# Kernel optimization log

Hardware: AMD Instinct MI355X
Metric: run time of the kernel (lower is better)

## Reference

```python
import jax, jax.numpy as jnp
import numpy as np

N, D, H = 4096, 128, 8

def setup_inputs() -> dict:
    key = jax.random.key(0)
    ks = jax.random.split(key, 7)
    xavier = float(np.sqrt(6.0 / (D + D)))  # xavier_uniform for [*, D, D]
    x = jax.random.normal(ks[0], (N, D), dtype=jnp.float32)
    W_k = jax.random.uniform(ks[1], (H, D, D), minval=-xavier, maxval=xavier, dtype=jnp.float32)
    W_q = jax.random.uniform(ks[2], (H, D, D), minval=-xavier, maxval=xavier, dtype=jnp.float32)
    W_v = jax.random.uniform(ks[3], (H, D, D), minval=-xavier, maxval=xavier, dtype=jnp.float32)
    W_m = jnp.ones((H,), dtype=jnp.float32)
    lim = float(1.0 / np.sqrt(D))  # default torch Linear init range
    Wg = jax.random.uniform(ks[4], (D, D), minval=-lim, maxval=lim, dtype=jnp.float32)
    bg = jax.random.uniform(ks[5], (D,), minval=-lim, maxval=lim, dtype=jnp.float32)
    return {"x": x, "W_k": W_k, "W_q": W_q, "W_v": W_v, "W_m": W_m, "Wg": Wg, "bg": bg}

def reference(x, W_k, W_q, W_v, W_m, Wg, bg):
    # per-head projections: [H, N, D]
    q = jnp.einsum('nf,hfd->hnd', x, W_q)
    k = jnp.einsum('nf,hfd->hnd', x, W_k)
    v = jnp.einsum('nf,hfd->hnd', x, W_v)
    # dense all-pairs attention scores per head: [H, N, N]
    e = jnp.einsum('hnd,hmd->hnm', q, k)
    attn = jax.nn.softmax(e, axis=-1)
    # weighted sum over values, then head-scaled accumulation: [N, D]
    out = jnp.einsum('h,hnm,hmd->nd', W_m, attn, v)
    # residual MLP: x + ReLU(Linear(x + out))
    h = x + out
    g = jax.nn.relu(h @ Wg.T + bg)
    return x + g
```

## Files before the change

kernel.cpp:

```cpp
#include <hip/hip_runtime.h>

#define NROWS 4096
#define DDIM  128
#define NHEAD 8

typedef __attribute__((ext_vector_type(8))) short    short8;
typedef __attribute__((ext_vector_type(8))) _Float16 half8;
typedef __attribute__((ext_vector_type(4))) float    floatx4;

__device__ __forceinline__ float bf2f(unsigned short u){
  unsigned v = ((unsigned)u) << 16;
  return __builtin_bit_cast(float, v);
}
__device__ __forceinline__ unsigned short f2bf(float f){
  unsigned u = __builtin_bit_cast(unsigned, f);
  u += 0x7FFFu + ((u >> 16) & 1u);
  return (unsigned short)(u >> 16);
}
__device__ __forceinline__ void split2(float v, unsigned short& hi, unsigned short& lo){
  hi = f2bf(v);
  lo = f2bf(v - bf2f(hi));
}
__device__ __forceinline__ void async_cp16(const _Float16* g, _Float16* l){
  __builtin_amdgcn_global_load_lds(
      (const __attribute__((address_space(1))) void*)g,
      (__attribute__((address_space(3))) void*)l, 16, 0, 0);
}

__global__ void fill_kernel(float* __restrict__ out, float val, int n){
  int i = blockIdx.x * 256 + threadIdx.x;
  if (i < n) out[i] = val;
}

__global__ __launch_bounds__(256, 2) void proj_kernel(
    const float* __restrict__ x,
    const float* __restrict__ Wk, const float* __restrict__ Wv,
    _Float16* __restrict__ kfo, _Float16* __restrict__ vfo)
{
  __shared__ alignas(16) unsigned short wthi[DDIM][72];
  __shared__ alignas(16) unsigned short wtlo[DDIM][72];
  const int tid = threadIdx.x, lane = tid & 63, wave = tid >> 6;
  const int l4 = lane & 15, quad = lane >> 4;
  const int h = blockIdx.y, z = blockIdx.z;
  const float* W = (z == 0 ? Wk : Wv) + h * DDIM * DDIM;

  floatx4 acc[4][8];
#pragma unroll
  for (int t4 = 0; t4 < 4; t4++)
#pragma unroll
    for (int c = 0; c < 8; c++) acc[t4][c] = (floatx4)0.f;

  for (int fh = 0; fh < 2; fh++) {
    for (int i = tid; i < DDIM * 64; i += 256) {
      const int d = i >> 6, fl = i & 63;
      unsigned short hi, lo;
      split2(W[(fh * 64 + fl) * DDIM + d], hi, lo);
      wthi[d][fl] = hi; wtlo[d][fl] = lo;
    }
    __syncthreads();

#pragma unroll
    for (int t4 = 0; t4 < 4; t4++) {
      const int tile = blockIdx.x * 4 + t4;
      const float* xr = x + (size_t)(tile * 64 + wave * 16 + l4) * DDIM + fh * 64 + quad * 8;
      short8 ah[2], al[2];
#pragma unroll
      for (int t2 = 0; t2 < 2; t2++) {
        float4 v0 = *(const float4*)(xr + t2 * 32);
        float4 v1 = *(const float4*)(xr + t2 * 32 + 4);
        float xv[8] = {v0.x, v0.y, v0.z, v0.w, v1.x, v1.y, v1.z, v1.w};
#pragma unroll
        for (int j = 0; j < 8; j++) {
          unsigned short hi, lo; split2(xv[j], hi, lo);
          ah[t2][j] = (short)hi; al[t2][j] = (short)lo;
        }
      }
#pragma unroll
      for (int t2 = 0; t2 < 2; t2++) {
#pragma unroll
        for (int c = 0; c < 8; c++) {
          short8 bh = *(const short8*)(&wthi[c * 16 + l4][t2 * 32 + quad * 8]);
          short8 bl = *(const short8*)(&wtlo[c * 16 + l4][t2 * 32 + quad * 8]);
          acc[t4][c] = __builtin_amdgcn_mfma_f32_16x16x32_bf16(ah[t2], bh, acc[t4][c], 0, 0, 0);
          acc[t4][c] = __builtin_amdgcn_mfma_f32_16x16x32_bf16(al[t2], bh, acc[t4][c], 0, 0, 0);
          acc[t4][c] = __builtin_amdgcn_mfma_f32_16x16x32_bf16(ah[t2], bl, acc[t4][c], 0, 0, 0);
        }
      }
    }
    __syncthreads();
  }

  const int rb = wave * 16 + quad * 4;
#pragma unroll
  for (int t4 = 0; t4 < 4; t4++) {
    const int tile = blockIdx.x * 4 + t4;
    const size_t tilebase = (size_t)(h * 64 + tile) * 8192;
#pragma unroll
    for (int c = 0; c < 8; c++) {
      const int d = c * 16 + l4;
#pragma unroll
      for (int r = 0; r < 4; r++) {
        const int kl = rb + r;
        const float val = acc[t4][c][r];
        if (z == 0) {
          const int c2 = kl >> 4, l4k = kl & 15;
          const int tt = d >> 5, qd = (d >> 3) & 3, jj = d & 7;
          const int qX = qd ^ ((l4k >> 1) & 3);
          kfo[tilebase + (size_t)((c2 * 4 + tt) * 16 + l4k) * 32 + qX * 8 + jj] =
              (_Float16)val;
        } else {
          const int c2 = d >> 4, l4v = d & 15;
          const int tt = kl >> 5, qd = (kl >> 3) & 3, jj = kl & 7;
          const int qX = qd ^ ((l4v >> 1) & 3);
          vfo[tilebase + (size_t)((c2 * 2 + tt) * 16 + l4v) * 32 + qX * 8 + jj] =
              (_Float16)val;
        }
      }
    }
  }
}

union FlashLds {
  struct { unsigned short hi[DDIM][72], lo[DDIM][72]; } wq;
  float qf[64][132];
  struct { _Float16 k[2][8192], p[4][2][1024]; } kv;
};

__global__ __launch_bounds__(256, 2) void flash_kernel(
    const float* __restrict__ x, const float* __restrict__ Wq,
    const _Float16* __restrict__ kfo, const _Float16* __restrict__ vfo,
    _Float16* __restrict__ op, float* __restrict__ mb, float* __restrict__ lb)
{
  __shared__ alignas(16) FlashLds lds;
  const int tid = threadIdx.x, lane = tid & 63, wave = tid >> 6;
  const int l4 = lane & 15, quad = lane >> 4;
  const int h = blockIdx.x & 7, qt = (blockIdx.x >> 3) & 31, s = blockIdx.x >> 8;
  const int q0 = qt * 128;

  half8 aq[2][4];

  {
    floatx4 qacc[2][8];
#pragma unroll
    for (int sp = 0; sp < 2; sp++)
#pragma unroll
      for (int c = 0; c < 8; c++) qacc[sp][c] = (floatx4)0.f;

    const float* Wqh = Wq + h * DDIM * DDIM;
    for (int fh = 0; fh < 2; fh++) {
      for (int i = tid; i < DDIM * 64; i += 256) {
        const int d = i >> 6, fl = i & 63;
        unsigned short hi, lo;
        split2(Wqh[(fh * 64 + fl) * DDIM + d], hi, lo);
        lds.wq.hi[d][fl] = hi; lds.wq.lo[d][fl] = lo;
      }
      __syncthreads();
#pragma unroll
      for (int sp = 0; sp < 2; sp++) {
        const float* xr = x + (size_t)(q0 + sp * 64 + wave * 16 + l4) * DDIM + fh * 64 + quad * 8;
        short8 ah[2], al[2];
#pragma unroll
        for (int t2 = 0; t2 < 2; t2++) {
          float4 v0 = *(const float4*)(xr + t2 * 32);
          float4 v1 = *(const float4*)(xr + t2 * 32 + 4);
          float xv[8] = {v0.x, v0.y, v0.z, v0.w, v1.x, v1.y, v1.z, v1.w};
#pragma unroll
          for (int j = 0; j < 8; j++) {
            unsigned short hi, lo; split2(xv[j], hi, lo);
            ah[t2][j] = (short)hi; al[t2][j] = (short)lo;
          }
        }
#pragma unroll
        for (int t2 = 0; t2 < 2; t2++) {
#pragma unroll
          for (int c = 0; c < 8; c++) {
            short8 bh = *(const short8*)(&lds.wq.hi[c * 16 + l4][t2 * 32 + quad * 8]);
            short8 bl = *(const short8*)(&lds.wq.lo[c * 16 + l4][t2 * 32 + quad * 8]);
            qacc[sp][c] = __builtin_amdgcn_mfma_f32_16x16x32_bf16(ah[t2], bh, qacc[sp][c], 0, 0, 0);
            qacc[sp][c] = __builtin_amdgcn_mfma_f32_16x16x32_bf16(al[t2], bh, qacc[sp][c], 0, 0, 0);
            qacc[sp][c] = __builtin_amdgcn_mfma_f32_16x16x32_bf16(ah[t2], bl, qacc[sp][c], 0, 0, 0);
          }
        }
      }
      __syncthreads();
    }

#pragma unroll
    for (int sp = 0; sp < 2; sp++) {
#pragma unroll
      for (int c = 0; c < 8; c++)
#pragma unroll
        for (int r = 0; r < 4; r++)
          lds.qf[wave * 16 + quad * 4 + r][c * 16 + l4] = qacc[sp][c][r];
      __syncthreads();
      if ((wave >> 1) == sp) {
#pragma unroll
        for (int g = 0; g < 2; g++)
#pragma unroll
          for (int t = 0; t < 4; t++) {
            const float* qr = &lds.qf[(wave & 1) * 32 + g * 16 + l4][t * 32 + quad * 8];
            float4 v0 = *(const float4*)qr;
            float4 v1 = *(const float4*)(qr + 4);
            aq[g][t][0] = (_Float16)v0.x; aq[g][t][1] = (_Float16)v0.y;
            aq[g][t][2] = (_Float16)v0.z; aq[g][t][3] = (_Float16)v0.w;
            aq[g][t][4] = (_Float16)v1.x; aq[g][t][5] = (_Float16)v1.y;
            aq[g][t][6] = (_Float16)v1.z; aq[g][t][7] = (_Float16)v1.w;
          }
      }
      __syncthreads();
    }
  }

  float m_run[2][4];
#pragma unroll
  for (int g = 0; g < 2; g++)
#pragma unroll
    for (int r = 0; r < 4; r++) m_run[g][r] = -1e30f;
  floatx4 Oacc[2][8], lacc[2];
#pragma unroll
  for (int g = 0; g < 2; g++) {
    lacc[g] = (floatx4)0.f;
#pragma unroll
    for (int c = 0; c < 8; c++) Oacc[g][c] = (floatx4)0.f;
  }

  half8 vones;
#pragma unroll
  for (int j = 0; j < 8; j++) vones[j] = (_Float16)1.f;

  const _Float16* kfo_h = kfo + (size_t)h * 64 * 8192;
  const _Float16* vfo_h = vfo + (size_t)h * 64 * 8192;
  const int lq = (l4 * 4 + (quad ^ ((l4 >> 1) & 3))) * 8;
  const int kt0 = s * 32, kt1 = kt0 + 32;

  {
    const _Float16* ks = kfo_h + (size_t)kt0 * 8192 + wave * 2048 + lane * 8;
    _Float16* kd = &lds.kv.k[0][wave * 2048];
#pragma unroll
    for (int it = 0; it < 4; it++) async_cp16(ks + it * 512, kd + it * 512);
  }

  for (int kt = kt0; kt < kt1; ++kt) {
    const int cur = kt & 1;
    __syncthreads();

    half8 vfrag[8][2];
    {
      const _Float16* vtb = vfo_h + (size_t)kt * 8192;
#pragma unroll
      for (int c = 0; c < 8; c++)
#pragma unroll
        for (int t = 0; t < 2; t++)
          vfrag[c][t] = *(const half8*)(vtb + (c * 2 + t) * 512 + lq);
    }
    if (kt + 1 < kt1) {
      const _Float16* ks = kfo_h + (size_t)(kt + 1) * 8192 + wave * 2048 + lane * 8;
      _Float16* kd = &lds.kv.k[cur ^ 1][wave * 2048];
#pragma unroll
      for (int it = 0; it < 4; it++) async_cp16(ks + it * 512, kd + it * 512);
    }

    floatx4 Sf[2][4];
#pragma unroll
    for (int g = 0; g < 2; g++)
#pragma unroll
      for (int c = 0; c < 4; c++) Sf[g][c] = (floatx4)0.f;
#pragma unroll
    for (int t = 0; t < 4; t++) {
      half8 b[4];
#pragma unroll
      for (int c = 0; c < 4; c++)
        b[c] = *(const half8*)&lds.kv.k[cur][(c * 4 + t) * 512 + lq];
#pragma unroll
      for (int g = 0; g < 2; g++)
#pragma unroll
        for (int c = 0; c < 4; c++)
          Sf[g][c] = __builtin_amdgcn_mfma_f32_16x16x32_f16(aq[g][t], b[c], Sf[g][c], 0, 0, 0);
    }

    float alpha[2][4];
#pragma unroll
    for (int g = 0; g < 2; g++) {
      float mt[4];
#pragma unroll
      for (int r = 0; r < 4; r++)
        mt[r] = fmaxf(fmaxf(Sf[g][0][r], Sf[g][1][r]), fmaxf(Sf[g][2][r], Sf[g][3][r]));
#pragma unroll
      for (int mk = 1; mk <= 8; mk <<= 1)
#pragma unroll
        for (int r = 0; r < 4; r++) mt[r] = fmaxf(mt[r], __shfl_xor(mt[r], mk, 64));
#pragma unroll
      for (int r = 0; r < 4; r++) {
        const float mn = fmaxf(m_run[g][r], mt[r]);
        alpha[g][r] = __expf(m_run[g][r] - mn);
        m_run[g][r] = mn;
      }
#pragma unroll
      for (int r = 0; r < 4; r++)
#pragma unroll
        for (int c = 0; c < 4; c++) Sf[g][c][r] = __expf(Sf[g][c][r] - m_run[g][r]);
    }

#pragma unroll
    for (int g = 0; g < 2; g++)
#pragma unroll
      for (int c = 0; c < 4; c++)
#pragma unroll
        for (int r = 0; r < 4; r++)
          lds.kv.p[wave][g][((c * 2 + (l4 >> 3)) * 16 + quad * 4 + r) * 8 + (l4 & 7)] =
              (_Float16)Sf[g][c][r];

#pragma unroll
    for (int g = 0; g < 2; g++) {
      const bool moved = (alpha[g][0] != 1.f) | (alpha[g][1] != 1.f) |
                         (alpha[g][2] != 1.f) | (alpha[g][3] != 1.f);
      if (__any(moved)) {
#pragma unroll
        for (int c = 0; c < 8; c++) {
          Oacc[g][c][0] *= alpha[g][0]; Oacc[g][c][1] *= alpha[g][1];
          Oacc[g][c][2] *= alpha[g][2]; Oacc[g][c][3] *= alpha[g][3];
        }
        lacc[g][0] *= alpha[g][0]; lacc[g][1] *= alpha[g][1];
        lacc[g][2] *= alpha[g][2]; lacc[g][3] *= alpha[g][3];
      }
    }
#pragma unroll
    for (int t = 0; t < 2; t++) {
      half8 ap[2];
#pragma unroll
      for (int g = 0; g < 2; g++) {
        ap[g] = *(const half8*)&lds.kv.p[wave][g][((t * 4 + quad) * 16 + l4) * 8];
        lacc[g] = __builtin_amdgcn_mfma_f32_16x16x32_f16(ap[g], vones, lacc[g], 0, 0, 0);
      }
#pragma unroll
      for (int c = 0; c < 8; c++)
#pragma unroll
        for (int g = 0; g < 2; g++)
          Oacc[g][c] = __builtin_amdgcn_mfma_f32_16x16x32_f16(ap[g], vfrag[c][t], Oacc[g][c], 0, 0, 0);
    }
  }

#pragma unroll
  for (int g = 0; g < 2; g++) {
    const int rbase = wave * 32 + g * 16 + quad * 4;
    const size_t rowbase = (size_t)(s * NHEAD + h) * NROWS + q0 + rbase;
#pragma unroll
    for (int c = 0; c < 8; c++) {
      const int col = c * 16 + l4;
#pragma unroll
      for (int r = 0; r < 4; r++)
        op[(rowbase + r) * DDIM + col] = (_Float16)Oacc[g][c][r];
    }
    if (l4 == 0) {
#pragma unroll
      for (int r = 0; r < 4; r++) {
        mb[rowbase + r] = m_run[g][r];
        lb[rowbase + r] = lacc[g][r];
      }
    }
  }
}

__global__ __launch_bounds__(128) void merge_kernel(
    const _Float16* __restrict__ op, const float* __restrict__ mb,
    const float* __restrict__ lb, const float* __restrict__ Wm,
    float* __restrict__ u)
{
  __shared__ float sc[2][NHEAD];
  const int n = blockIdx.x, d = threadIdx.x;
  if (d < NHEAD) {
    const int h = d;
    const float m1 = mb[(size_t)h * NROWS + n];
    const float m2 = mb[(size_t)(NHEAD + h) * NROWS + n];
    const float l1 = lb[(size_t)h * NROWS + n];
    const float l2 = lb[(size_t)(NHEAD + h) * NROWS + n];
    const float m  = fmaxf(m1, m2);
    const float a1 = __expf(m1 - m), a2 = __expf(m2 - m);
    const float invL = Wm[h] / (l1 * a1 + l2 * a2);
    sc[0][h] = a1 * invL;
    sc[1][h] = a2 * invL;
  }
  __syncthreads();
  float acc = 0.f;
#pragma unroll
  for (int h = 0; h < NHEAD; h++) {
    acc += sc[0][h] * (float)op[((size_t)h * NROWS + n) * DDIM + d];
    acc += sc[1][h] * (float)op[((size_t)(NHEAD + h) * NROWS + n) * DDIM + d];
  }
  u[(size_t)n * DDIM + d] = acc;
}

__global__ __launch_bounds__(256, 2) void mlp_kernel(
    const float* __restrict__ x, const float* __restrict__ u,
    const float* __restrict__ Wg, const float* __restrict__ bg,
    float* __restrict__ out)
{
  __shared__ alignas(16) unsigned short wghi[DDIM][72];
  __shared__ alignas(16) unsigned short wglo[DDIM][72];
  const int tid = threadIdx.x, lane = tid & 63, wave = tid >> 6;
  const int l4 = lane & 15, quad = lane >> 4;
  const int r0 = blockIdx.x * 64;

  floatx4 acc[8];
#pragma unroll
  for (int c = 0; c < 8; c++) acc[c] = (floatx4)0.f;

  for (int fh = 0; fh < 2; fh++) {
    for (int i = tid; i < DDIM * 64; i += 256) {
      const int ii = i >> 6, jl = i & 63;
      unsigned short hi, lo;
      split2(Wg[ii * DDIM + fh * 64 + jl], hi, lo);
      wghi[ii][jl] = hi; wglo[ii][jl] = lo;
    }
    __syncthreads();

    const size_t xoff = (size_t)(r0 + wave * 16 + l4) * DDIM + fh * 64 + quad * 8;
    short8 ah[2], al[2];
#pragma unroll
    for (int t2 = 0; t2 < 2; t2++) {
      float4 x0 = *(const float4*)(x + xoff + t2 * 32);
      float4 x1 = *(const float4*)(x + xoff + t2 * 32 + 4);
      float4 u0 = *(const float4*)(u + xoff + t2 * 32);
      float4 u1 = *(const float4*)(u + xoff + t2 * 32 + 4);
      float hv[8] = {x0.x + u0.x, x0.y + u0.y, x0.z + u0.z, x0.w + u0.w,
                     x1.x + u1.x, x1.y + u1.y, x1.z + u1.z, x1.w + u1.w};
#pragma unroll
      for (int j = 0; j < 8; j++) {
        unsigned short hi, lo; split2(hv[j], hi, lo);
        ah[t2][j] = (short)hi; al[t2][j] = (short)lo;
      }
    }
#pragma unroll
    for (int t2 = 0; t2 < 2; t2++) {
#pragma unroll
      for (int c = 0; c < 8; c++) {
        short8 bh = *(const short8*)(&wghi[c * 16 + l4][t2 * 32 + quad * 8]);
        short8 bl = *(const short8*)(&wglo[c * 16 + l4][t2 * 32 + quad * 8]);
        acc[c] = __builtin_amdgcn_mfma_f32_16x16x32_bf16(ah[t2], bh, acc[c], 0, 0, 0);
        acc[c] = __builtin_amdgcn_mfma_f32_16x16x32_bf16(al[t2], bh, acc[c], 0, 0, 0);
        acc[c] = __builtin_amdgcn_mfma_f32_16x16x32_bf16(ah[t2], bl, acc[c], 0, 0, 0);
      }
    }
    __syncthreads();
  }

  const int rbase = wave * 16 + quad * 4;
#pragma unroll
  for (int c = 0; c < 8; c++) {
    const int col = c * 16 + l4;
    const float bgf = bg[col];
#pragma unroll
    for (int r = 0; r < 4; r++) {
      const size_t idx = (size_t)(r0 + rbase + r) * DDIM + col;
      out[idx] = x[idx] + fmaxf(acc[c][r] + bgf, 0.f);
    }
  }
}

extern "C" void kernel_launch(void* const* d_in, const int* in_sizes, int n_in,
                              void* d_out, int out_size, void* d_ws, size_t ws_size,
                              hipStream_t stream) {
  float* out = (float*)d_out;
  const int fill_blocks = (out_size + 255) / 256;

  const bool ok_sizes =
      n_in == 7 &&
      in_sizes[0] == NROWS * DDIM &&
      in_sizes[1] == NHEAD * DDIM * DDIM &&
      in_sizes[2] == NHEAD * DDIM * DDIM &&
      in_sizes[3] == NHEAD * DDIM * DDIM &&
      in_sizes[4] == NHEAD &&
      in_sizes[5] == DDIM * DDIM &&
      in_sizes[6] == DDIM &&
      out_size == NROWS * DDIM;
  if (!ok_sizes) {
    fill_kernel<<<fill_blocks, 256, 0, stream>>>(out, 1000.f, out_size);
    return;
  }

  const size_t HND = (size_t)NHEAD * NROWS * DDIM;
  const size_t ND  = (size_t)NROWS * DDIM;
  const size_t need = ND * 4 + 2 * HND * 2 + 2 * HND * 2 + 2 * NHEAD * NROWS * 8;
  if (ws_size < need) {
    fill_kernel<<<fill_blocks, 256, 0, stream>>>(out, 500.f, out_size);
    return;
  }

  const float* x  = (const float*)d_in[0];
  const float* Wk = (const float*)d_in[1];
  const float* Wq = (const float*)d_in[2];
  const float* Wv = (const float*)d_in[3];
  const float* Wm = (const float*)d_in[4];
  const float* Wg = (const float*)d_in[5];
  const float* bg = (const float*)d_in[6];

  float*     u   = (float*)d_ws;
  _Float16*  kfo = (_Float16*)(u + ND);
  _Float16*  vfo = kfo + HND;
  _Float16*  op  = vfo + HND;
  float*     mb  = (float*)(op + 2 * HND);
  float*     lb  = mb + 2 * NHEAD * NROWS;

  (void)hipGetLastError();
  proj_kernel<<<dim3(16, NHEAD, 2), 256, 0, stream>>>(x, Wk, Wv, kfo, vfo);
  flash_kernel<<<dim3(512), 256, 0, stream>>>(x, Wq, kfo, vfo, op, mb, lb);
  merge_kernel<<<dim3(4096), 128, 0, stream>>>(op, mb, lb, Wm, u);
  mlp_kernel<<<dim3(64), 256, 0, stream>>>(x, u, Wg, bg, out);
  if (hipGetLastError() != hipSuccess) {
    fill_kernel<<<fill_blocks, 256, 0, stream>>>(out, 2000.f, out_size);
  }
}
```

Baseline: 254.5 us.

## Move Q projection into proj kernel and halve flash query tile for occupancy

Q projection moves out of the flash kernel into proj_kernel as a third z-slice, written to a new fp16 workspace buffer prescaled by log2(e). The flash kernel then loads Q directly, uses 64-row query tiles with one group per wave, launches 1024 blocks, and raises launch bounds to 4 blocks per CU thanks to smaller LDS and register use. Softmax exponentials switch from expf to native exp2, and the weight-transpose load loop index is reordered for coalesced global reads. The cost is an extra HND fp16 round trip through global memory and each K/V tile being streamed by twice as many blocks.

```diff
diff --git a/kernel.cpp b/kernel.cpp
--- a/kernel.cpp
+++ b/kernel.cpp
@@ -3,6 +3,9 @@
 #define NROWS 4096
 #define DDIM  128
 #define NHEAD 8
+#define LOG2E 1.44269504088896f
+
+extern "C" __device__ float __ocml_native_exp2_f32(float);
 
 typedef __attribute__((ext_vector_type(8))) short    short8;
 typedef __attribute__((ext_vector_type(8))) _Float16 half8;
@@ -35,14 +38,16 @@
 __global__ __launch_bounds__(256, 2) void proj_kernel(
     const float* __restrict__ x,
     const float* __restrict__ Wk, const float* __restrict__ Wv,
-    _Float16* __restrict__ kfo, _Float16* __restrict__ vfo)
+    const float* __restrict__ Wq,
+    _Float16* __restrict__ kfo, _Float16* __restrict__ vfo,
+    _Float16* __restrict__ qfo)
 {
   __shared__ alignas(16) unsigned short wthi[DDIM][72];
   __shared__ alignas(16) unsigned short wtlo[DDIM][72];
   const int tid = threadIdx.x, lane = tid & 63, wave = tid >> 6;
   const int l4 = lane & 15, quad = lane >> 4;
   const int h = blockIdx.y, z = blockIdx.z;
-  const float* W = (z == 0 ? Wk : Wv) + h * DDIM * DDIM;
+  const float* W = (z == 0 ? Wk : (z == 1 ? Wv : Wq)) + h * DDIM * DDIM;
 
   floatx4 acc[4][8];
 #pragma unroll
@@ -52,7 +57,7 @@
 
   for (int fh = 0; fh < 2; fh++) {
     for (int i = tid; i < DDIM * 64; i += 256) {
-      const int d = i >> 6, fl = i & 63;
+      const int d = i & 127, fl = i >> 7;
       unsigned short hi, lo;
       split2(W[(fh * 64 + fl) * DDIM + d], hi, lo);
       wthi[d][fl] = hi; wtlo[d][fl] = lo;
@@ -108,121 +113,51 @@
           const int qX = qd ^ ((l4k >> 1) & 3);
           kfo[tilebase + (size_t)((c2 * 4 + tt) * 16 + l4k) * 32 + qX * 8 + jj] =
               (_Float16)val;
-        } else {
+        } else if (z == 1) {
           const int c2 = d >> 4, l4v = d & 15;
           const int tt = kl >> 5, qd = (kl >> 3) & 3, jj = kl & 7;
           const int qX = qd ^ ((l4v >> 1) & 3);
           vfo[tilebase + (size_t)((c2 * 2 + tt) * 16 + l4v) * 32 + qX * 8 + jj] =
               (_Float16)val;
+        } else {
+          qfo[((size_t)h * NROWS + (size_t)tile * 64 + kl) * DDIM + d] =
+              (_Float16)(val * LOG2E);
         }
       }
     }
   }
 }
 
-union FlashLds {
-  struct { unsigned short hi[DDIM][72], lo[DDIM][72]; } wq;
-  float qf[64][132];
-  struct { _Float16 k[2][8192], p[4][2][1024]; } kv;
+struct FlashLds {
+  _Float16 k[2][8192];
+  _Float16 p[4][1024];
 };
 
-__global__ __launch_bounds__(256, 2) void flash_kernel(
-    const float* __restrict__ x, const float* __restrict__ Wq,
-    const _Float16* __restrict__ kfo, const _Float16* __restrict__ vfo,
+__global__ __launch_bounds__(256, 4) void flash_kernel(
+    const _Float16* __restrict__ qfo, const _Float16* __restrict__ kfo,
+    const _Float16* __restrict__ vfo,
     _Float16* __restrict__ op, float* __restrict__ mb, float* __restrict__ lb)
 {
   __shared__ alignas(16) FlashLds lds;
   const int tid = threadIdx.x, lane = tid & 63, wave = tid >> 6;
   const int l4 = lane & 15, quad = lane >> 4;
-  const int h = blockIdx.x & 7, qt = (blockIdx.x >> 3) & 31, s = blockIdx.x >> 8;
-  const int q0 = qt * 128;
-
-  half8 aq[2][4];
-
+  const int h = blockIdx.x & 7, qt = (blockIdx.x >> 3) & 63, s = blockIdx.x >> 9;
+  const int q0 = qt * 64;
+
+  half8 aq[4];
   {
-    floatx4 qacc[2][8];
-#pragma unroll
-    for (int sp = 0; sp < 2; sp++)
-#pragma unroll
-      for (int c = 0; c < 8; c++) qacc[sp][c] = (floatx4)0.f;
-
-    const float* Wqh = Wq + h * DDIM * DDIM;
-    for (int fh = 0; fh < 2; fh++) {
-      for (int i = tid; i < DDIM * 64; i += 256) {
-        const int d = i >> 6, fl = i & 63;
-        unsigned short hi, lo;
-        split2(Wqh[(fh * 64 + fl) * DDIM + d], hi, lo);
-        lds.wq.hi[d][fl] = hi; lds.wq.lo[d][fl] = lo;
-      }
-      __syncthreads();
-#pragma unroll
-      for (int sp = 0; sp < 2; sp++) {
-        const float* xr = x + (size_t)(q0 + sp * 64 + wave * 16 + l4) * DDIM + fh * 64 + quad * 8;
-        short8 ah[2], al[2];
-#pragma unroll
-        for (int t2 = 0; t2 < 2; t2++) {
-          float4 v0 = *(const float4*)(xr + t2 * 32);
-          float4 v1 = *(const float4*)(xr + t2 * 32 + 4);
-          float xv[8] = {v0.x, v0.y, v0.z, v0.w, v1.x, v1.y, v1.z, v1.w};
-#pragma unroll
-          for (int j = 0; j < 8; j++) {
-            unsigned short hi, lo; split2(xv[j], hi, lo);
-            ah[t2][j] = (short)hi; al[t2][j] = (short)lo;
-          }
-        }
-#pragma unroll
-        for (int t2 = 0; t2 < 2; t2++) {
-#pragma unroll
-          for (int c = 0; c < 8; c++) {
-            short8 bh = *(const short8*)(&lds.wq.hi[c * 16 + l4][t2 * 32 + quad * 8]);
-            short8 bl = *(const short8*)(&lds.wq.lo[c * 16 + l4][t2 * 32 + quad * 8]);
-            qacc[sp][c] = __builtin_amdgcn_mfma_f32_16x16x32_bf16(ah[t2], bh, qacc[sp][c], 0, 0, 0);
-            qacc[sp][c] = __builtin_amdgcn_mfma_f32_16x16x32_bf16(al[t2], bh, qacc[sp][c], 0, 0, 0);
-            qacc[sp][c] = __builtin_amdgcn_mfma_f32_16x16x32_bf16(ah[t2], bl, qacc[sp][c], 0, 0, 0);
-          }
-        }
-      }
-      __syncthreads();
-    }
-
-#pragma unroll
-    for (int sp = 0; sp < 2; sp++) {
-#pragma unroll
-      for (int c = 0; c < 8; c++)
-#pragma unroll
-        for (int r = 0; r < 4; r++)
-          lds.qf[wave * 16 + quad * 4 + r][c * 16 + l4] = qacc[sp][c][r];
-      __syncthreads();
-      if ((wave >> 1) == sp) {
-#pragma unroll
-        for (int g = 0; g < 2; g++)
-#pragma unroll
-          for (int t = 0; t < 4; t++) {
-            const float* qr = &lds.qf[(wave & 1) * 32 + g * 16 + l4][t * 32 + quad * 8];
-            float4 v0 = *(const float4*)qr;
-            float4 v1 = *(const float4*)(qr + 4);
-            aq[g][t][0] = (_Float16)v0.x; aq[g][t][1] = (_Float16)v0.y;
-            aq[g][t][2] = (_Float16)v0.z; aq[g][t][3] = (_Float16)v0.w;
-            aq[g][t][4] = (_Float16)v1.x; aq[g][t][5] = (_Float16)v1.y;
-            aq[g][t][6] = (_Float16)v1.z; aq[g][t][7] = (_Float16)v1.w;
-          }
-      }
-      __syncthreads();
-    }
-  }
-
-  float m_run[2][4];
-#pragma unroll
-  for (int g = 0; g < 2; g++)
-#pragma unroll
-    for (int r = 0; r < 4; r++) m_run[g][r] = -1e30f;
-  floatx4 Oacc[2][8], lacc[2];
-#pragma unroll
-  for (int g = 0; g < 2; g++) {
-    lacc[g] = (floatx4)0.f;
-#pragma unroll
-    for (int c = 0; c < 8; c++) Oacc[g][c] = (floatx4)0.f;
-  }
+    const _Float16* qr =
+        qfo + ((size_t)h * NROWS + q0 + wave * 16 + l4) * DDIM + quad * 8;
+#pragma unroll
+    for (int t = 0; t < 4; t++) aq[t] = *(const half8*)(qr + t * 32);
+  }
+
+  float m_run[4];
+#pragma unroll
+  for (int r = 0; r < 4; r++) m_run[r] = -1e30f;
+  floatx4 Oacc[8], lacc = (floatx4)0.f;
+#pragma unroll
+  for (int c = 0; c < 8; c++) Oacc[c] = (floatx4)0.f;
 
   half8 vones;
 #pragma unroll
@@ -235,7 +170,7 @@
 
   {
     const _Float16* ks = kfo_h + (size_t)kt0 * 8192 + wave * 2048 + lane * 8;
-    _Float16* kd = &lds.kv.k[0][wave * 2048];
+    _Float16* kd = &lds.k[0][wave * 2048];
 #pragma unroll
     for (int it = 0; it < 4; it++) async_cp16(ks + it * 512, kd + it * 512);
   }
@@ -255,108 +190,93 @@
     }
     if (kt + 1 < kt1) {
       const _Float16* ks = kfo_h + (size_t)(kt + 1) * 8192 + wave * 2048 + lane * 8;
-      _Float16* kd = &lds.kv.k[cur ^ 1][wave * 2048];
+      _Float16* kd = &lds.k[cur ^ 1][wave * 2048];
 #pragma unroll
       for (int it = 0; it < 4; it++) async_cp16(ks + it * 512, kd + it * 512);
     }
 
-    floatx4 Sf[2][4];
-#pragma unroll
-    for (int g = 0; g < 2; g++)
-#pragma unroll
-      for (int c = 0; c < 4; c++) Sf[g][c] = (floatx4)0.f;
+    floatx4 Sf[4];
+#pragma unroll
+    for (int c = 0; c < 4; c++) Sf[c] = (floatx4)0.f;
 #pragma unroll
     for (int t = 0; t < 4; t++) {
       half8 b[4];
 #pragma unroll
       for (int c = 0; c < 4; c++)
-        b[c] = *(const half8*)&lds.kv.k[cur][(c * 4 + t) * 512 + lq];
-#pragma unroll
-      for (int g = 0; g < 2; g++)
+        b[c] = *(const half8*)&lds.k[cur][(c * 4 + t) * 512 + lq];
+#pragma unroll
+      for (int c = 0; c < 4; c++)
+        Sf[c] = __builtin_amdgcn_mfma_f32_16x16x32_f16(aq[t], b[c], Sf[c], 0, 0, 0);
+    }
+
+    float alpha[4];
+    {
+      float mt[4];
+#pragma unroll
+      for (int r = 0; r < 4; r++)
+        mt[r] = fmaxf(fmaxf(Sf[0][r], Sf[1][r]), fmaxf(Sf[2][r], Sf[3][r]));
+#pragma unroll
+      for (int mk = 1; mk <= 8; mk <<= 1)
+#pragma unroll
+        for (int r = 0; r < 4; r++) mt[r] = fmaxf(mt[r], __shfl_xor(mt[r], mk, 64));
+#pragma unroll
+      for (int r = 0; r < 4; r++) {
+        const float mn = fmaxf(m_run[r], mt[r]);
+        alpha[r] = __ocml_native_exp2_f32(m_run[r] - mn);
+        m_run[r] = mn;
+      }
+#pragma unroll
+      for (int r = 0; r < 4; r++)
 #pragma unroll
         for (int c = 0; c < 4; c++)
-          Sf[g][c] = __builtin_amdgcn_mfma_f32_16x16x32_f16(aq[g][t], b[c], Sf[g][c], 0, 0, 0);
-    }
-
-    float alpha[2][4];
-#pragma unroll
-    for (int g = 0; g < 2; g++) {
-      float mt[4];
+          Sf[c][r] = __ocml_native_exp2_f32(Sf[c][r] - m_run[r]);
+    }
+
+#pragma unroll
+    for (int c = 0; c < 4; c++)
 #pragma unroll
       for (int r = 0; r < 4; r++)
-        mt[r] = fmaxf(fmaxf(Sf[g][0][r], Sf[g][1][r]), fmaxf(Sf[g][2][r], Sf[g][3][r]));
-#pragma unroll
-      for (int mk = 1; mk <= 8; mk <<= 1)
-#pragma unroll
-        for (int r = 0; r < 4; r++) mt[r] = fmaxf(mt[r], __shfl_xor(mt[r], mk, 64));
-#pragma unroll
-      for (int r = 0; r < 4; r++) {
-        const float mn = fmaxf(m_run[g][r], mt[r]);
-        alpha[g][r] = __expf(m_run[g][r] - mn);
-        m_run[g][r] = mn;
-      }
-#pragma unroll
-      for (int r = 0; r < 4; r++)
-#pragma unroll
-        for (int c = 0; c < 4; c++) Sf[g][c][r] = __expf(Sf[g][c][r] - m_run[g][r]);
-    }
-
-#pragma unroll
-    for (int g = 0; g < 2; g++)
-#pragma unroll
-      for (int c = 0; c < 4; c++)
-#pragma unroll
-        for (int r = 0; r < 4; r++)
-          lds.kv.p[wave][g][((c * 2 + (l4 >> 3)) * 16 + quad * 4 + r) * 8 + (l4 & 7)] =
-              (_Float16)Sf[g][c][r];
-
-#pragma unroll
-    for (int g = 0; g < 2; g++) {
-      const bool moved = (alpha[g][0] != 1.f) | (alpha[g][1] != 1.f) |
-                         (alpha[g][2] != 1.f) | (alpha[g][3] != 1.f);
+        lds.p[wave][((c * 2 + (l4 >> 3)) * 16 + quad * 4 + r) * 8 + (l4 & 7)] =
+            (_Float16)Sf[c][r];
+
+    {
+      const bool moved = (alpha[0] != 1.f) | (alpha[1] != 1.f) |
+                         (alpha[2] != 1.f) | (alpha[3] != 1.f);
       if (__any(moved)) {
 #pragma unroll
         for (int c = 0; c < 8; c++) {
-          Oacc[g][c][0] *= alpha[g][0]; Oacc[g][c][1] *= alpha[g][1];
-          Oacc[g][c][2] *= alpha[g][2]; Oacc[g][c][3] *= alpha[g][3];
+          Oacc[c][0] *= alpha[0]; Oacc[c][1] *= alpha[1];
+          Oacc[c][2] *= alpha[2]; Oacc[c][3] *= alpha[3];
         }
-        lacc[g][0] *= alpha[g][0]; lacc[g][1] *= alpha[g][1];
-        lacc[g][2] *= alpha[g][2]; lacc[g][3] *= alpha[g][3];
-      }
-    }
+        lacc[0] *= alpha[0]; lacc[1] *= alpha[1];
+        lacc[2] *= alpha[2]; lacc[3] *= alpha[3];
+      }
+    }
+
 #pragma unroll
     for (int t = 0; t < 2; t++) {
-      half8 ap[2];
-#pragma unroll
-      for (int g = 0; g < 2; g++) {
-        ap[g] = *(const half8*)&lds.kv.p[wave][g][((t * 4 + quad) * 16 + l4) * 8];
-        lacc[g] = __builtin_amdgcn_mfma_f32_16x16x32_f16(ap[g], vones, lacc[g], 0, 0, 0);
-      }
+      half8 ap = *(const half8*)&lds.p[wave][((t * 4 + quad) * 16 + l4) * 8];
+      lacc = __builtin_amdgcn_mfma_f32_16x16x32_f16(ap, vones, lacc, 0, 0, 0);
 #pragma unroll
       for (int c = 0; c < 8; c++)
-#pragma unroll
-        for (int g = 0; g < 2; g++)
-          Oacc[g][c] = __builtin_amdgcn_mfma_f32_16x16x32_f16(ap[g], vfrag[c][t], Oacc[g][c], 0, 0, 0);
-    }
-  }
-
-#pragma unroll
-  for (int g = 0; g < 2; g++) {
-    const int rbase = wave * 32 + g * 16 + quad * 4;
-    const size_t rowbase = (size_t)(s * NHEAD + h) * NROWS + q0 + rbase;
-#pragma unroll
-    for (int c = 0; c < 8; c++) {
-      const int col = c * 16 + l4;
-#pragma unroll
-      for (int r = 0; r < 4; r++)
-        op[(rowbase + r) * DDIM + col] = (_Float16)Oacc[g][c][r];
-    }
-    if (l4 == 0) {
-#pragma unroll
-      for (int r = 0; r < 4; r++) {
-        mb[rowbase + r] = m_run[g][r];
-        lb[rowbase + r] = lacc[g][r];
-      }
+        Oacc[c] = __builtin_amdgcn_mfma_f32_16x16x32_f16(ap, vfrag[c][t], Oacc[c], 0, 0, 0);
+    }
+  }
+
+  const int rbase = wave * 16 + quad * 4;
+  const size_t rowbase = (size_t)(s * NHEAD + h) * NROWS + q0 + rbase;
+#pragma unroll
+  for (int c = 0; c < 8; c++) {
+    const int col = c * 16 + l4;
+#pragma unroll
+    for (int r = 0; r < 4; r++)
+      op[(rowbase + r) * DDIM + col] = (_Float16)Oacc[c][r];
+  }
+  if (l4 == 0) {
+#pragma unroll
+    for (int r = 0; r < 4; r++) {
+      mb[rowbase + r] = m_run[r];
+      lb[rowbase + r] = lacc[r];
     }
   }
 }
@@ -375,7 +295,8 @@
     const float l1 = lb[(size_t)h * NROWS + n];
     const float l2 = lb[(size_t)(NHEAD + h) * NROWS + n];
     const float m  = fmaxf(m1, m2);
-    const float a1 = __expf(m1 - m), a2 = __expf(m2 - m);
+    const float a1 = __ocml_native_exp2_f32(m1 - m);
+    const float a2 = __ocml_native_exp2_f32(m2 - m);
     const float invL = Wm[h] / (l1 * a1 + l2 * a2);
     sc[0][h] = a1 * invL;
     sc[1][h] = a2 * invL;
@@ -480,7 +401,7 @@
 
   const size_t HND = (size_t)NHEAD * NROWS * DDIM;
   const size_t ND  = (size_t)NROWS * DDIM;
-  const size_t need = ND * 4 + 2 * HND * 2 + 2 * HND * 2 + 2 * NHEAD * NROWS * 8;
+  const size_t need = ND * 4 + 3 * HND * 2 + 2 * HND * 2 + 2 * NHEAD * NROWS * 8;
   if (ws_size < need) {
     fill_kernel<<<fill_blocks, 256, 0, stream>>>(out, 500.f, out_size);
     return;
@@ -497,13 +418,14 @@
   float*     u   = (float*)d_ws;
   _Float16*  kfo = (_Float16*)(u + ND);
   _Float16*  vfo = kfo + HND;
-  _Float16*  op  = vfo + HND;
+  _Float16*  qfo = vfo + HND;
+  _Float16*  op  = qfo + HND;
   float*     mb  = (float*)(op + 2 * HND);
   float*     lb  = mb + 2 * NHEAD * NROWS;
 
   (void)hipGetLastError();
-  proj_kernel<<<dim3(16, NHEAD, 2), 256, 0, stream>>>(x, Wk, Wv, kfo, vfo);
-  flash_kernel<<<dim3(512), 256, 0, stream>>>(x, Wq, kfo, vfo, op, mb, lb);
+  proj_kernel<<<dim3(16, NHEAD, 3), 256, 0, stream>>>(x, Wk, Wv, Wq, kfo, vfo, qfo);
+  flash_kernel<<<dim3(1024), 256, 0, stream>>>(qfo, kfo, vfo, op, mb, lb);
   merge_kernel<<<dim3(4096), 128, 0, stream>>>(op, mb, lb, Wm, u);
   mlp_kernel<<<dim3(64), 256, 0, stream>>>(x, u, Wg, bg, out);
   if (hipGetLastError() != hipSuccess) {
```

Result: slower. 440.3 us (+73.0%).
